# Kernel optimization log

Measured on AMD Instinct MI355X. Metric: run time of the kernel, lower is better.

Reference implementation:

```python
import jax, jax.numpy as jnp
import numpy as np

B, C, T = 4, 80, 800            # batch, n_mels (= d_model), frames
DEPTH, D_IN, N, DT_R, K = 12, 160, 16, 5, 4  # layers, expand*d_model, d_state, dt_rank, conv kernel
ATT, EMB, EPS = 128, 192, 1e-12

LP_NAMES = ['ln1_g','ln1_b','in_proj','conv_w','conv_b','x_proj','dt_w','dt_b','A_log','D','out_proj','ln2_g','ln2_b','ff_w1','ff_b1','ff_w2','ff_b2']
PP_NAMES = ['att_w1','att_b1','bn1_g','bn1_b','bn1_m','bn1_v','att_w2','att_b2','bn2_g','bn2_b','bn2_m','bn2_v','fc_w','fc_b']


def _layernorm(x, g, b, eps=1e-5):
    mu = x.mean(-1, keepdims=True)
    v = ((x - mu) ** 2).mean(-1, keepdims=True)
    return (x - mu) * jax.lax.rsqrt(v + eps) * g + b


def _mamba(x, p):
    # x: [B, L, d_model] -> standard Mamba selective-scan block
    xz = x @ p['in_proj']                              # [B,L,2*D_IN]
    xc, z = jnp.split(xz, 2, axis=-1)
    xp = jnp.pad(xc, ((0, 0), (K - 1, 0), (0, 0)))     # causal left pad
    xc = jax.lax.conv_general_dilated(
        xp, p['conv_w'], (1,), 'VALID',
        dimension_numbers=('NWC', 'WIO', 'NWC'),
        feature_group_count=D_IN) + p['conv_b']
    xc = jax.nn.silu(xc)
    dbc = xc @ p['x_proj']                             # [B,L,DT_R+2N]
    dt, Bm, Cm = jnp.split(dbc, [DT_R, DT_R + N], axis=-1)
    dt = jax.nn.softplus(dt @ p['dt_w'] + p['dt_b'])   # [B,L,D_IN]
    A = -jnp.exp(p['A_log'])                           # [D_IN,N]

    def step(h, inp):
        x_t, dt_t, B_t, C_t = inp                      # [B,D],[B,D],[B,N],[B,N]
        dA = jnp.exp(dt_t[..., None] * A)              # [B,D,N]
        h = dA * h + (dt_t * x_t)[..., None] * B_t[:, None, :]
        y = jnp.einsum('bdn,bn->bd', h, C_t)
        return h, y

    h0 = jnp.zeros((x.shape[0], D_IN, N), x.dtype)
    xs = tuple(jnp.swapaxes(a, 0, 1) for a in (xc, dt, Bm, Cm))
    _, ys = jax.lax.scan(step, h0, xs)
    y = jnp.swapaxes(ys, 0, 1) + xc * p['D']
    y = y * jax.nn.silu(z)
    return y @ p['out_proj']


def _encoder(x, p):
    xn = _layernorm(x, p['ln1_g'], p['ln1_b'])
    fwd = _mamba(xn, p)
    bwd = jnp.flip(_mamba(jnp.flip(xn, 1), p), 1)      # bidirectional, shared weights
    m = _layernorm(fwd + bwd, p['ln2_g'], p['ln2_b'])
    ff = jax.nn.gelu(m @ p['ff_w1'] + p['ff_b1'], approximate=False) @ p['ff_w2'] + p['ff_b2']
    return ff + x


def _forward(feat, lp, pp):
    feat = feat - feat.mean(-1, keepdims=True)         # CMN
    x = jnp.swapaxes(feat, 1, 2)                       # [B,T,C]

    def body(xc, p):
        return _encoder(xc, p), None

    x, _ = jax.lax.scan(body, x, lp)                   # 12 stacked layers
    x = jnp.swapaxes(x, 1, 2)                          # [B,C,T]

    # Attentive statistics pooling (global context)
    mean = x.mean(-1, keepdims=True)
    std = jnp.sqrt(jnp.maximum(((x - mean) ** 2).mean(-1, keepdims=True), EPS))
    g = jnp.concatenate([x, jnp.broadcast_to(mean, x.shape), jnp.broadcast_to(std, x.shape)], axis=1)  # [B,3C,T]
    a = jnp.einsum('bct,cd->bdt', g, pp['att_w1']) + pp['att_b1'][:, None]
    a = jax.nn.relu(a)
    a = (a - pp['bn1_m'][:, None]) * jax.lax.rsqrt(pp['bn1_v'][:, None] + 1e-5) * pp['bn1_g'][:, None] + pp['bn1_b'][:, None]
    a = jnp.tanh(a)
    a = jnp.einsum('bdt,dc->bct', a, pp['att_w2']) + pp['att_b2'][:, None]
    w = jax.nn.softmax(a, axis=-1)
    mu = jnp.sum(w * x, axis=-1)
    sg = jnp.sqrt(jnp.maximum(jnp.sum(w * x * x, axis=-1) - mu ** 2, EPS))
    pooled = jnp.concatenate([mu, sg], axis=-1)        # [B,2C]

    pooled = (pooled - pp['bn2_m']) * jax.lax.rsqrt(pp['bn2_v'] + 1e-5) * pp['bn2_g'] + pp['bn2_b']
    return pooled @ pp['fc_w'] + pp['fc_b']            # [B,EMB] source embedding


def setup_inputs() -> dict:
    key = jax.random.key(0)
    ks = jax.random.split(key, 12)

    def w(k, shape, s=0.05):
        return jax.random.normal(k, shape, jnp.float32) * s

    L = DEPTH
    return {
        'feat': jax.random.normal(ks[0], (B, C, T), jnp.float32),
        'ln1_g': jnp.ones((L, C)), 'ln1_b': jnp.zeros((L, C)),
        'in_proj': w(ks[1], (L, C, 2 * D_IN)),
        'conv_w': w(ks[2], (L, K, 1, D_IN), 0.2),
        'conv_b': jnp.zeros((L, D_IN)),
        'x_proj': w(ks[3], (L, D_IN, DT_R + 2 * N)),
        'dt_w': w(ks[4], (L, DT_R, D_IN), 0.2),
        'dt_b': jnp.full((L, D_IN), -2.0),
        'A_log': jnp.tile(jnp.log(jnp.arange(1, N + 1, dtype=jnp.float32)), (L, D_IN, 1)),
        'D': jnp.ones((L, D_IN)),
        'out_proj': w(ks[5], (L, D_IN, C)),
        'ln2_g': jnp.ones((L, C)), 'ln2_b': jnp.zeros((L, C)),
        'ff_w1': w(ks[6], (L, C, 4 * C)), 'ff_b1': jnp.zeros((L, 4 * C)),
        'ff_w2': w(ks[7], (L, 4 * C, C)), 'ff_b2': jnp.zeros((L, C)),
        'att_w1': w(ks[8], (3 * C, ATT)), 'att_b1': jnp.zeros((ATT,)),
        'bn1_g': jnp.ones((ATT,)), 'bn1_b': jnp.zeros((ATT,)),
        'bn1_m': jnp.zeros((ATT,)), 'bn1_v': jnp.ones((ATT,)),
        'att_w2': w(ks[9], (ATT, C)), 'att_b2': jnp.zeros((C,)),
        'bn2_g': jnp.ones((2 * C,)), 'bn2_b': jnp.zeros((2 * C,)),
        'bn2_m': jnp.zeros((2 * C,)), 'bn2_v': jnp.ones((2 * C,)),
        'fc_w': w(ks[10], (2 * C, EMB)), 'fc_b': jnp.zeros((EMB,)),
        'aug': 0,
    }


def reference(feat, ln1_g, ln1_b, in_proj, conv_w, conv_b, x_proj, dt_w, dt_b, A_log, D, out_proj, ln2_g, ln2_b, ff_w1, ff_b1, ff_w2, ff_b2, att_w1, att_b1, bn1_g, bn1_b, bn1_m, bn1_v, att_w2, att_b2, bn2_g, bn2_b, bn2_m, bn2_v, fc_w, fc_b, aug):
    lp = dict(zip(LP_NAMES, (ln1_g, ln1_b, in_proj, conv_w, conv_b, x_proj, dt_w, dt_b, A_log, D, out_proj, ln2_g, ln2_b, ff_w1, ff_b1, ff_w2, ff_b2)))
    pp = dict(zip(PP_NAMES, (att_w1, att_b1, bn1_g, bn1_b, bn1_m, bn1_v, att_w2, att_b2, bn2_g, bn2_b, bn2_m, bn2_v, fc_w, fc_b)))
    # aug == 0 -> SpecAug skipped (eval path); speaker branch (frozen, no_grad) omitted
    return _forward(feat, lp, pp)
```

## Files before the change

### kernel.cpp

```cpp
#include <hip/hip_runtime.h>
#include <hip/hip_bf16.h>

#define B_ 4
#define C_ 80
#define T_ 800
#define R_ 3200
#define DIN 160
#define NST 16
#define NC 16
#define LCH 50

typedef const float* fp;

__device__ __forceinline__ void g2l16(const float* g, float* l) {
  __builtin_amdgcn_global_load_lds(
      (const __attribute__((address_space(1))) void*)g,
      (__attribute__((address_space(3))) void*)l,
      16, 0, 0);
}

__device__ __forceinline__ float blockSum(float v, float* sb) {
  for (int o = 32; o; o >>= 1) v += __shfl_xor(v, o);
  __syncthreads();
  if ((threadIdx.x & 63) == 0) sb[threadIdx.x >> 6] = v;
  __syncthreads();
  return sb[0] + sb[1] + sb[2] + sb[3];
}
__device__ __forceinline__ float blockMax(float v, float* sb) {
  for (int o = 32; o; o >>= 1) v = fmaxf(v, __shfl_xor(v, o));
  __syncthreads();
  if ((threadIdx.x & 63) == 0) sb[threadIdx.x >> 6] = v;
  __syncthreads();
  return fmaxf(fmaxf(sb[0], sb[1]), fmaxf(sb[2], sb[3]));
}

__global__ __launch_bounds__(256) void prepw_k(fp in_proj, fp ff_w1,
    fp ln1_g, fp ln1_b, fp ln2_g, fp ln2_b, fp ff_b1,
    float* __restrict__ wp, float* __restrict__ uvb) {
  int idx = blockIdx.x * 256 + threadIdx.x;
  int c = idx % 320, lm = idx / 320;
  int mat = lm & 1, l = lm >> 1;
  fp W = (mat ? ff_w1 : in_proj) + l * 25600;
  fp g = (mat ? ln2_g : ln1_g) + l * 80;
  fp b = (mat ? ln2_b : ln1_b) + l * 80;
  float* wpo = wp + lm * 25600;
  float u = 0.f, v = 0.f;
  for (int k = 0; k < 80; ++k) {
    float w = W[k * 320 + c];
    float gw = g[k] * w;
    wpo[k * 320 + c] = gw;
    u += gw;
    v += b[k] * w;
  }
  if (mat) v += ff_b1[l * 320 + c];
  uvb[lm * 640 + c] = u;
  uvb[lm * 640 + 320 + c] = v;
}

__global__ __launch_bounds__(256) void prepx_k(fp x_proj, float* __restrict__ xpt) {
  int idx = blockIdx.x * 256 + threadIdx.x;
  if (idx >= 71040) return;
  int l = idx / 5920, r = idx % 5920;
  int c = r / 160, k = r % 160;
  xpt[idx] = x_proj[l * 5920 + k * 37 + c];
}

__global__ __launch_bounds__(256) void cmn_k(fp feat, float* __restrict__ x) {
  int bc = blockIdx.x;
  int b = bc / C_, c = bc % C_;
  const float* f = feat + (b * C_ + c) * T_;
  __shared__ float sb[4];
  int tid = threadIdx.x;
  float v[4]; float s = 0.f;
  #pragma unroll
  for (int i = 0; i < 4; ++i) {
    int t = tid + i * 256;
    v[i] = (t < T_) ? f[t] : 0.f;
    s += v[i];
  }
  s = blockSum(s, sb);
  float mu = s * (1.f / T_);
  #pragma unroll
  for (int i = 0; i < 4; ++i) {
    int t = tid + i * 256;
    if (t < T_) x[(b * T_ + t) * C_ + c] = v[i] - mu;
  }
}

__global__ __launch_bounds__(256) void rstat_k(const float* __restrict__ in,
                                               float* __restrict__ must) {
  int row = blockIdx.x * 16 + (threadIdx.x >> 4);
  int c16 = threadIdx.x & 15;
  float s = 0.f, q = 0.f;
  #pragma unroll
  for (int m = 0; m < 5; ++m) {
    float v = in[row * 80 + c16 + 16 * m];
    s += v; q += v * v;
  }
  s += __shfl_xor(s, 1); s += __shfl_xor(s, 2);
  s += __shfl_xor(s, 4); s += __shfl_xor(s, 8);
  q += __shfl_xor(q, 1); q += __shfl_xor(q, 2);
  q += __shfl_xor(q, 4); q += __shfl_xor(q, 8);
  if (c16 == 0) {
    float mu = s * 0.0125f;
    float rs = rsqrtf(fmaxf(q * 0.0125f - mu * mu, 0.f) + 1e-5f);
    must[row * 2] = mu;
    must[row * 2 + 1] = rs;
  }
}

template<int EPI>
__global__ __launch_bounds__(256, 4) void gw_k(const float* __restrict__ A,
    fp W, fp uv, const float* __restrict__ must, const float* __restrict__ extra,
    float* __restrict__ out, int N) {
  __shared__ float SL[5120 + 4 * 1280];
  int tid = threadIdx.x, wv = tid >> 6, ln = tid & 63;
  int bid = blockIdx.x;
  int c0 = (bid / 50) * 64;
  int row0 = ((bid % 50) * 4 + wv) * 16;
  for (int ch = wv; ch < 20; ch += 4) {
    int m = ch * 256 + ln * 4;
    int kr = m >> 6, cc = m & 63;
    int lo = __builtin_amdgcn_readfirstlane(ch * 256);
    g2l16(W + kr * N + c0 + cc, SL + lo);
  }
  int abase = __builtin_amdgcn_readfirstlane(5120 + wv * 1280);
  float* As = SL + 5120 + wv * 1280;
  #pragma unroll
  for (int i = 0; i < 5; ++i) {
    int m = i * 256 + ln * 4;
    int r = m / 80, kk = m - r * 80;
    g2l16(A + (row0 + r) * 80 + kk, SL + abase + i * 256);
  }
  __syncthreads();
  int rq = ln >> 4, c16 = ln & 15;
  float acc[4][4] = {};
  #pragma unroll 2
  for (int k4 = 0; k4 < 80; k4 += 4) {
    float4 a[4], w[4];
    #pragma unroll
    for (int i = 0; i < 4; ++i)
      a[i] = *(const float4*)&As[(rq * 4 + i) * 80 + k4];
    #pragma unroll
    for (int kk = 0; kk < 4; ++kk)
      w[kk] = *(const float4*)&SL[(k4 + kk) * 64 + c16 * 4];
    #pragma unroll
    for (int i = 0; i < 4; ++i) {
      acc[i][0] += a[i].x*w[0].x + a[i].y*w[1].x + a[i].z*w[2].x + a[i].w*w[3].x;
      acc[i][1] += a[i].x*w[0].y + a[i].y*w[1].y + a[i].z*w[2].y + a[i].w*w[3].y;
      acc[i][2] += a[i].x*w[0].z + a[i].y*w[1].z + a[i].z*w[2].z + a[i].w*w[3].z;
      acc[i][3] += a[i].x*w[0].w + a[i].y*w[1].w + a[i].z*w[2].w + a[i].w*w[3].w;
    }
  }
  float ua[4], va[4];
  if (EPI != 3) {
    *(float4*)ua = *(const float4*)&uv[c0 + c16 * 4];
    *(float4*)va = *(const float4*)&uv[N + c0 + c16 * 4];
  }
  #pragma unroll
  for (int i = 0; i < 4; ++i) {
    int row = row0 + rq * 4 + i;
    float mu = 0.f, rs = 1.f;
    if (EPI != 3) {
      float2 ms = *(const float2*)&must[row * 2];
      mu = ms.x; rs = ms.y;
    }
    float4 o;
    float* op = &o.x;
    #pragma unroll
    for (int j = 0; j < 4; ++j) {
      float v = acc[i][j];
      if (EPI == 3) {
        int c = c0 + c16 * 4 + j;
        v += extra[(row / T_) * 128 + c];
        v = fmaxf(v, 0.f);
        v = v * extra[512 + c] + extra[640 + c];
        v = tanhf(v);
      } else {
        v = rs * v - mu * rs * ua[j] + va[j];
        if (EPI == 1) v = 0.5f * v * (1.f + erff(v * 0.70710678118f));
      }
      op[j] = v;
    }
    *(float4*)&out[row * N + c0 + c16 * 4] = o;
  }
}

template<int EPI, int KCH, int NKC, int SUM2, int STAT>
__global__ __launch_bounds__(256, 4) void gc_k(const float* __restrict__ A,
    fp W, fp bias, const float* __restrict__ extra, float* __restrict__ out,
    int Astride, float* __restrict__ must) {
  constexpr int P = KCH + 4;
  __shared__ float As[16 * P];
  __shared__ float Wt[80 * P];
  int tid = threadIdx.x;
  int row0 = blockIdx.x * 16;
  int rr = tid >> 4, c16 = tid & 15;
  float acc[5] = {};
  for (int kc = 0; kc < NKC; ++kc) {
    if (kc) __syncthreads();
    #pragma unroll
    for (int i = 0; i < 16 * KCH / 256; ++i) {
      int e = tid + i * 256;
      int r = e / KCH, k = e - r * KCH;
      float v;
      if (SUM2) v = A[(row0 + r) * 320 + k] + A[(row0 + r) * 320 + 160 + k];
      else      v = A[(row0 + r) * Astride + kc * KCH + k];
      As[r * P + k] = v;
    }
    #pragma unroll
    for (int i = 0; i < KCH * 80 / 256; ++i) {
      int e = tid + i * 256;
      int kr = e / 80, c = e - kr * 80;
      Wt[c * P + kr] = W[(kc * KCH + kr) * 80 + c];
    }
    __syncthreads();
    #pragma unroll 4
    for (int k4 = 0; k4 < KCH; k4 += 4) {
      float4 a = *(const float4*)&As[rr * P + k4];
      #pragma unroll
      for (int m = 0; m < 5; ++m) {
        float4 w = *(const float4*)&Wt[(c16 + 16 * m) * P + k4];
        acc[m] += a.x * w.x + a.y * w.y + a.z * w.z + a.w * w.w;
      }
    }
  }
  int row = row0 + rr;
  float s = 0.f, q = 0.f;
  #pragma unroll
  for (int m = 0; m < 5; ++m) {
    int c = c16 + 16 * m;
    float v = acc[m];
    if (EPI == 2) v += bias[c] + extra[row * 80 + c];
    else if (EPI == 4) v += bias[c];
    out[row * 80 + c] = v;
    if (STAT) { s += v; q += v * v; }
  }
  if (STAT) {
    s += __shfl_xor(s, 1); s += __shfl_xor(s, 2);
    s += __shfl_xor(s, 4); s += __shfl_xor(s, 8);
    q += __shfl_xor(q, 1); q += __shfl_xor(q, 2);
    q += __shfl_xor(q, 4); q += __shfl_xor(q, 8);
    if (c16 == 0) {
      float mu = s * 0.0125f;
      float rs = rsqrtf(fmaxf(q * 0.0125f - mu * mu, 0.f) + 1e-5f);
      must[row * 2] = mu;
      must[row * 2 + 1] = rs;
    }
  }
}

__global__ __launch_bounds__(256) void cxf_k(const float* __restrict__ xz,
    fp cw, fp cb, fp xptl, fp dtw, fp dtb,
    float* __restrict__ xcf, float* __restrict__ xcbb,
    float* __restrict__ dbc2, float* __restrict__ dt2) {
  __shared__ float As[16 * 164];
  __shared__ float dbcl[16 * 40];
  int bi = blockIdx.x;
  int tc = bi % 50; int rem = bi / 50;
  int b = rem & 3, dir = rem >> 2;
  int t0 = tc * 16;
  int tid = threadIdx.x;
  float* xco = dir ? xcbb : xcf;
  #pragma unroll
  for (int i = 0; i < 3; ++i) {
    int e = tid + i * 256;
    if (e < 640) {
      int ii = e / 40, d4 = (e - ii * 40) * 4;
      int t = t0 + ii;
      float4 acc = *(const float4*)&cb[d4];
      #pragma unroll
      for (int k = 0; k < 4; ++k) {
        int tt = t - 3 + k;
        if (tt >= 0) {
          int src = dir ? (T_ - 1 - tt) : tt;
          float4 xv = *(const float4*)&xz[(b * T_ + src) * 320 + d4];
          float4 wv = *(const float4*)&cw[k * DIN + d4];
          acc.x += wv.x * xv.x; acc.y += wv.y * xv.y;
          acc.z += wv.z * xv.z; acc.w += wv.w * xv.w;
        }
      }
      float4 o;
      o.x = acc.x / (1.f + __expf(-acc.x));
      o.y = acc.y / (1.f + __expf(-acc.y));
      o.z = acc.z / (1.f + __expf(-acc.z));
      o.w = acc.w / (1.f + __expf(-acc.w));
      *(float4*)&As[ii * 164 + d4] = o;
      *(float4*)&xco[(b * T_ + t) * DIN + d4] = o;
    }
  }
  __syncthreads();
  int rr = tid >> 4, c16 = tid & 15;
  int grow0 = dir * R_ + b * T_ + t0;
  {
    float a0 = 0.f, a1 = 0.f, a2 = 0.f;
    for (int k4 = 0; k4 < 160; k4 += 4) {
      float4 a = *(const float4*)&As[rr * 164 + k4];
      float4 w0 = *(const float4*)&xptl[c16 * 160 + k4];
      float4 w1 = *(const float4*)&xptl[(c16 + 16) * 160 + k4];
      a0 += a.x * w0.x + a.y * w0.y + a.z * w0.z + a.w * w0.w;
      a1 += a.x * w1.x + a.y * w1.y + a.z * w1.z + a.w * w1.w;
      if (c16 < 5) {
        float4 w2 = *(const float4*)&xptl[(c16 + 32) * 160 + k4];
        a2 += a.x * w2.x + a.y * w2.y + a.z * w2.z + a.w * w2.w;
      }
    }
    dbcl[rr * 40 + c16] = a0;
    dbcl[rr * 40 + c16 + 16] = a1;
    dbc2[(grow0 + rr) * 37 + c16] = a0;
    dbc2[(grow0 + rr) * 37 + c16 + 16] = a1;
    if (c16 < 5) {
      dbcl[rr * 40 + c16 + 32] = a2;
      dbc2[(grow0 + rr) * 37 + c16 + 32] = a2;
    }
  }
  __syncthreads();
  #pragma unroll
  for (int i = 0; i < 10; ++i) {
    int e = tid + i * 256;
    int ii = e / 160, d = e - ii * 160;
    float v = dtb[d];
    #pragma unroll
    for (int m = 0; m < 5; ++m) v += dbcl[ii * 40 + m] * dtw[m * DIN + d];
    v = fmaxf(v, 0.f) + log1pf(expf(-fabsf(v)));
    dt2[(grow0 + ii) * DIN + d] = v;
  }
}

__global__ __launch_bounds__(256) void scanA_k(const float* __restrict__ dt2,
    const float* __restrict__ xcf, const float* __restrict__ xcbb,
    const float* __restrict__ dbc2, fp A_log,
    float* __restrict__ hend, float* __restrict__ pprod) {
  int bi = blockIdx.x;
  int cch = bi % NC; int rem = bi / NC;
  int dblk = rem % 10; rem /= 10;
  int b = rem % 4; int dir = rem / 4;
  int d0 = dblk * 16;
  int tid = threadIdx.x, dl = tid >> 4, n = tid & 15;
  int d = d0 + dl;
  float Areg = -__expf(A_log[d * NST + n]);
  __shared__ float sdt[LCH][16], sdx[LCH][16], sB[LCH][16];
  const float* xc = dir ? xcbb : xcf;
  int rbase = dir * R_ + b * T_ + cch * LCH;
  int rloc0 = b * T_ + cch * LCH;
  for (int e = tid; e < LCH * 16; e += 256) {
    int i = e >> 4, jj = e & 15;
    int grow = rbase + i;
    float dtv = dt2[grow * DIN + d0 + jj];
    sdt[i][jj] = dtv;
    sdx[i][jj] = dtv * xc[(rloc0 + i) * DIN + d0 + jj];
    sB[i][jj]  = dbc2[grow * 37 + 5 + jj];
  }
  __syncthreads();
  float h = 0.f, dts = 0.f;
  #pragma unroll 2
  for (int i = 0; i < LCH; ++i) {
    float dtv = sdt[i][dl];
    float a = __expf(dtv * Areg);
    h = a * h + sdx[i][dl] * sB[i][n];
    dts += dtv;
  }
  hend[bi * 256 + tid] = h;
  pprod[bi * 256 + tid] = __expf(dts * Areg);
}

__global__ __launch_bounds__(256) void scanC_k(const float* __restrict__ dt2,
    const float* __restrict__ dbc2, const float* __restrict__ xcf,
    const float* __restrict__ xcbb, const float* __restrict__ xz,
    fp A_log, fp Dp, const float* __restrict__ hend,
    const float* __restrict__ pprod, float* __restrict__ ygcat) {
  int bi = blockIdx.x;
  int cch = bi % NC; int rem = bi / NC;
  int dblk = rem % 10; rem /= 10;
  int b = rem % 4; int dir = rem / 4;
  int d0 = dblk * 16;
  int tid = threadIdx.x, dl = tid >> 4, n = tid & 15;
  int d = d0 + dl;
  float Areg = -__expf(A_log[d * NST + n]);
  __shared__ float sdt[LCH][16], sdx[LCH][16], sB[LCH][16], sC[LCH][16];
  __shared__ float sY[LCH][16];
  const float* xc = dir ? xcbb : xcf;
  int rbase = dir * R_ + b * T_ + cch * LCH;
  int rloc0 = b * T_ + cch * LCH;
  int sbase = (bi / NC) * (NC * 256) + tid;
  float h = 0.f;
  #pragma unroll
  for (int cc = 0; cc < NC; ++cc) {
    float p = pprod[sbase + cc * 256];
    float e = hend[sbase + cc * 256];
    if (cc < cch) h = p * h + e;
  }
  for (int e = tid; e < LCH * 16; e += 256) {
    int i = e >> 4, jj = e & 15;
    int grow = rbase + i;
    float dtv = dt2[grow * DIN + d0 + jj];
    sdt[i][jj] = dtv;
    sdx[i][jj] = dtv * xc[(rloc0 + i) * DIN + d0 + jj];
    sB[i][jj]  = dbc2[grow * 37 + 5 + jj];
    sC[i][jj]  = dbc2[grow * 37 + 21 + jj];
  }
  __syncthreads();
  for (int i = 0; i < LCH; ++i) {
    float a = __expf(sdt[i][dl] * Areg);
    h = a * h + sdx[i][dl] * sB[i][n];
    float y = h * sC[i][n];
    y += __shfl_xor(y, 1);
    y += __shfl_xor(y, 2);
    y += __shfl_xor(y, 4);
    y += __shfl_xor(y, 8);
    if (n == 0) sY[i][dl] = y;
  }
  __syncthreads();
  for (int e = tid; e < LCH * 16; e += 256) {
    int i = e >> 4, jj = e & 15;
    int t = cch * LCH + i;
    int rloc = b * T_ + t;
    float xcv = xc[rloc * DIN + d0 + jj];
    int orow = dir ? (b * T_ + (T_ - 1 - t)) : rloc;
    float z = xz[orow * 320 + 160 + d0 + jj];
    float sg = 1.f / (1.f + __expf(-z));
    ygcat[orow * 320 + dir * 160 + d0 + jj] = (sY[i][jj] + xcv * Dp[d0 + jj]) * (z * sg);
  }
}

__global__ __launch_bounds__(256) void stats_k(const float* __restrict__ x,
                                               float* __restrict__ meanv, float* __restrict__ stdv) {
  int bc = blockIdx.x; int b = bc / C_, c = bc % C_;
  __shared__ float sb[4];
  int tid = threadIdx.x;
  float v[4]; float s = 0.f;
  #pragma unroll
  for (int i = 0; i < 4; ++i) {
    int t = tid + i * 256;
    v[i] = (t < T_) ? x[(b * T_ + t) * C_ + c] : 0.f;
    s += v[i];
  }
  s = blockSum(s, sb);
  float mu = s * (1.f / T_);
  float q = 0.f;
  #pragma unroll
  for (int i = 0; i < 4; ++i) {
    int t = tid + i * 256;
    if (t < T_) { float dd = v[i] - mu; q += dd * dd; }
  }
  q = blockSum(q, sb);
  if (tid == 0) { meanv[bc] = mu; stdv[bc] = sqrtf(fmaxf(q * (1.f / T_), 1e-12f)); }
}

__global__ __launch_bounds__(256) void prep_k(const float* __restrict__ meanv,
    const float* __restrict__ stdv, fp w1, fp ab1, fp g1p, fp b1p, fp m1p, fp v1p,
    float* __restrict__ pack) {
  int idx = blockIdx.x * 256 + threadIdx.x;
  if (idx < 512) {
    int b = idx / 128, dcol = idx % 128;
    float acc = ab1[dcol];
    for (int c = 0; c < C_; ++c) {
      acc += meanv[b * C_ + c] * w1[(C_ + c) * 128 + dcol];
      acc += stdv[b * C_ + c] * w1[(2 * C_ + c) * 128 + dcol];
    }
    pack[idx] = acc;
  } else if (idx < 640) {
    int dcol = idx - 512;
    float kv = g1p[dcol] * rsqrtf(v1p[dcol] + 1e-5f);
    pack[512 + dcol] = kv;
    pack[640 + dcol] = b1p[dcol] - m1p[dcol] * kv;
  }
}

__global__ __launch_bounds__(256) void pool_k(const float* __restrict__ x,
    const float* __restrict__ scores, fp g2, fp b2, fp m2, fp v2,
    float* __restrict__ pooledn) {
  int bc = blockIdx.x; int b = bc / C_, c = bc % C_;
  __shared__ float sb[4];
  int tid = threadIdx.x;
  float sv[4], xv[4];
  float mx = -1e30f;
  #pragma unroll
  for (int i = 0; i < 4; ++i) {
    int t = tid + i * 256;
    if (t < T_) { sv[i] = scores[(b * T_ + t) * C_ + c]; xv[i] = x[(b * T_ + t) * C_ + c]; }
    else { sv[i] = -1e30f; xv[i] = 0.f; }
    mx = fmaxf(mx, sv[i]);
  }
  mx = blockMax(mx, sb);
  float se = 0.f, sx = 0.f, sxx = 0.f;
  #pragma unroll
  for (int i = 0; i < 4; ++i) {
    float e = expf(sv[i] - mx);
    se += e; sx += e * xv[i]; sxx += e * xv[i] * xv[i];
  }
  se = blockSum(se, sb);
  sx = blockSum(sx, sb);
  sxx = blockSum(sxx, sb);
  if (tid == 0) {
    float mu = sx / se;
    float sg = sqrtf(fmaxf(sxx / se - mu * mu, 1e-12f));
    int j0 = c, j1 = C_ + c;
    pooledn[b * 160 + j0] = (mu - m2[j0]) * rsqrtf(v2[j0] + 1e-5f) * g2[j0] + b2[j0];
    pooledn[b * 160 + j1] = (sg - m2[j1]) * rsqrtf(v2[j1] + 1e-5f) * g2[j1] + b2[j1];
  }
}

__global__ __launch_bounds__(256) void fc_k(const float* __restrict__ pooledn, fp fw, fp fb,
                                            float* __restrict__ out) {
  int idx = blockIdx.x * 256 + threadIdx.x;
  if (idx >= 4 * 192) return;
  int b = idx / 192, e = idx % 192;
  float acc = fb[e];
  for (int i = 0; i < 160; ++i) acc += pooledn[b * 160 + i] * fw[i * 192 + e];
  out[idx] = acc;
}

extern "C" void kernel_launch(void* const* d_in, const int* in_sizes, int n_in,
                              void* d_out, int out_size, void* d_ws, size_t ws_size,
                              hipStream_t stream) {
  fp feat   = (fp)d_in[0];
  fp ln1_g  = (fp)d_in[1];  fp ln1_b  = (fp)d_in[2];
  fp in_proj= (fp)d_in[3];
  fp conv_w = (fp)d_in[4];  fp conv_b = (fp)d_in[5];
  fp x_proj = (fp)d_in[6];
  fp dt_w   = (fp)d_in[7];  fp dt_b   = (fp)d_in[8];
  fp A_log  = (fp)d_in[9];  fp Dp     = (fp)d_in[10];
  fp out_proj=(fp)d_in[11];
  fp ln2_g  = (fp)d_in[12]; fp ln2_b  = (fp)d_in[13];
  fp ff_w1  = (fp)d_in[14]; fp ff_b1  = (fp)d_in[15];
  fp ff_w2  = (fp)d_in[16]; fp ff_b2  = (fp)d_in[17];
  fp att_w1 = (fp)d_in[18]; fp att_b1 = (fp)d_in[19];
  fp bn1_g  = (fp)d_in[20]; fp bn1_b  = (fp)d_in[21];
  fp bn1_m  = (fp)d_in[22]; fp bn1_v  = (fp)d_in[23];
  fp att_w2 = (fp)d_in[24]; fp att_b2 = (fp)d_in[25];
  fp bn2_g  = (fp)d_in[26]; fp bn2_b  = (fp)d_in[27];
  fp bn2_m  = (fp)d_in[28]; fp bn2_v  = (fp)d_in[29];
  fp fc_w   = (fp)d_in[30]; fp fc_b   = (fp)d_in[31];

  float* ws   = (float*)d_ws;
  float* x    = ws;
  float* xz   = ws + 256000;
  float* xcf  = ws + 1280000;
  float* xcb  = ws + 1792000;
  float* dbc2 = ws + 2304000;
  float* dt2  = ws + 2540800;
  float* hend = ws + 3564800;
  float* pprod= ws + 3892480;
  float* ygcat= ws + 4220160;
  float* sbuf = ws + 5244160;
  float* meanv= ws + 5500160;
  float* stdv = ws + 5500480;
  float* pack = ws + 5500800;
  float* pooledn = ws + 5501568;
  float* wp   = ws + 5502208;
  float* uvb  = ws + 6116608;
  float* mst_x= ws + 6131968;
  float* mst_s= ws + 6138368;
  float* xpt  = ws + 6144768;
  float* g1   = xz;
  float* a1b  = hend;
  float* sc   = dt2;

  prepw_k<<<30, 256, 0, stream>>>(in_proj, ff_w1, ln1_g, ln1_b, ln2_g, ln2_b,
                                  ff_b1, wp, uvb);
  prepx_k<<<278, 256, 0, stream>>>(x_proj, xpt);
  cmn_k<<<320, 256, 0, stream>>>(feat, x);
  rstat_k<<<200, 256, 0, stream>>>(x, mst_x);

  for (int l = 0; l < 12; ++l) {
    gw_k<0><<<250, 256, 0, stream>>>(x, wp + (2 * l) * 25600, uvb + (2 * l) * 640,
                                     mst_x, nullptr, xz, 320);
    cxf_k<<<400, 256, 0, stream>>>(xz, conv_w + l * 640, conv_b + l * 160,
                                   xpt + l * 5920, dt_w + l * 800, dt_b + l * 160,
                                   xcf, xcb, dbc2, dt2);
    scanA_k<<<1280, 256, 0, stream>>>(dt2, xcf, xcb, dbc2, A_log + l * 2560, hend, pprod);
    scanC_k<<<1280, 256, 0, stream>>>(dt2, dbc2, xcf, xcb, xz, A_log + l * 2560,
                                      Dp + l * 160, hend, pprod, ygcat);
    gc_k<0, 160, 1, 1, 1><<<200, 256, 0, stream>>>(ygcat, out_proj + l * 12800,
                                                   nullptr, nullptr, sbuf, 320, mst_s);
    gw_k<1><<<250, 256, 0, stream>>>(sbuf, wp + (2 * l + 1) * 25600,
                                     uvb + (2 * l + 1) * 640, mst_s, nullptr, g1, 320);
    gc_k<2, 160, 2, 0, 1><<<200, 256, 0, stream>>>(g1, ff_w2 + l * 25600,
                                                   ff_b2 + l * 80, x, x, 320, mst_x);
  }

  stats_k<<<320, 256, 0, stream>>>(x, meanv, stdv);
  prep_k<<<3, 256, 0, stream>>>(meanv, stdv, att_w1, att_b1, bn1_g, bn1_b, bn1_m, bn1_v, pack);
  gw_k<3><<<100, 256, 0, stream>>>(x, att_w1, nullptr, nullptr, pack, a1b, 128);
  gc_k<4, 128, 1, 0, 0><<<200, 256, 0, stream>>>(a1b, att_w2, att_b2, nullptr, sc, 128, nullptr);
  pool_k<<<320, 256, 0, stream>>>(x, sc, bn2_g, bn2_b, bn2_m, bn2_v, pooledn);
  fc_k<<<3, 256, 0, stream>>>(pooledn, fc_w, fc_b, (float*)d_out);
}
```

Measured before the change: 1.377 ms.

## Fuse per-layer GEMM chain into two kernels and stage x_proj weights in LDS

Replaces the per-layer out_proj, ff_w1 and ff_w2 plus next-layer in_proj kernels with two fused kernels. gof_k runs out_proj, LayerNorm2 statistics and ff_w1 with GELU. gfi_k runs ff_w2 with the residual, LayerNorm1 statistics and the next layer's in_proj, so intermediate rows and statistics stay in LDS. This cuts launches and global round-trips. Weights are pre-transposed once up front, cxf_k stages the x_proj weights in shared memory, and the softplus now uses fast intrinsics. In exchange the fused kernels use large LDS tiles at lower occupancy, and there is a small precision change in softplus.

```diff
diff --git a/kernel.cpp b/kernel.cpp
--- a/kernel.cpp
+++ b/kernel.cpp
@@ -65,6 +65,21 @@
   xpt[idx] = x_proj[l * 5920 + k * 37 + c];
 }
 
+__global__ __launch_bounds__(256) void prept_k(fp out_proj, fp ff_w2,
+    float* __restrict__ wot, float* __restrict__ w2t) {
+  int idx = blockIdx.x * 256 + threadIdx.x;
+  if (idx < 153600) {
+    int l = idx / 12800, r = idx % 12800;
+    int c = r / 160, k = r % 160;
+    wot[idx] = out_proj[l * 12800 + k * 80 + c];
+  } else if (idx < 153600 + 307200) {
+    int j = idx - 153600;
+    int l = j / 25600, r = j % 25600;
+    int c = r / 320, k = r % 320;
+    w2t[j] = ff_w2[l * 25600 + k * 80 + c];
+  }
+}
+
 __global__ __launch_bounds__(256) void cmn_k(fp feat, float* __restrict__ x) {
   int bc = blockIdx.x;
   int b = bc / C_, c = bc % C_;
@@ -178,7 +193,6 @@
         v = tanhf(v);
       } else {
         v = rs * v - mu * rs * ua[j] + va[j];
-        if (EPI == 1) v = 0.5f * v * (1.f + erff(v * 0.70710678118f));
       }
       op[j] = v;
     }
@@ -226,7 +240,6 @@
     }
   }
   int row = row0 + rr;
-  float s = 0.f, q = 0.f;
   #pragma unroll
   for (int m = 0; m < 5; ++m) {
     int c = c16 + 16 * m;
@@ -234,18 +247,158 @@
     if (EPI == 2) v += bias[c] + extra[row * 80 + c];
     else if (EPI == 4) v += bias[c];
     out[row * 80 + c] = v;
-    if (STAT) { s += v; q += v * v; }
-  }
-  if (STAT) {
+  }
+}
+
+__global__ __launch_bounds__(256, 2) void gof_k(const float* __restrict__ yg,
+    fp wotl, fp w1pl, fp uv1, float* __restrict__ g1) {
+  __shared__ float As[16 * 164];
+  __shared__ float Wt[80 * 164];
+  __shared__ float sl[16 * 84];
+  __shared__ float ss[32];
+  int tid = threadIdx.x, row0 = blockIdx.x * 16, rr = tid >> 4, c16 = tid & 15;
+  #pragma unroll
+  for (int i = 0; i < 10; ++i) {
+    int e = tid + i * 256; int r = e / 160, k = e - r * 160;
+    As[r * 164 + k] = yg[(row0 + r) * 320 + k] + yg[(row0 + r) * 320 + 160 + k];
+  }
+  #pragma unroll
+  for (int i = 0; i < 50; ++i) {
+    int e = tid + i * 256; int c = e / 160, k = e - c * 160;
+    Wt[c * 164 + k] = wotl[e];
+  }
+  __syncthreads();
+  float acc[5] = {};
+  #pragma unroll 4
+  for (int k4 = 0; k4 < 160; k4 += 4) {
+    float4 a = *(const float4*)&As[rr * 164 + k4];
+    #pragma unroll
+    for (int m = 0; m < 5; ++m) {
+      float4 w = *(const float4*)&Wt[(c16 + 16 * m) * 164 + k4];
+      acc[m] += a.x * w.x + a.y * w.y + a.z * w.z + a.w * w.w;
+    }
+  }
+  float s = 0.f, q = 0.f;
+  #pragma unroll
+  for (int m = 0; m < 5; ++m) {
+    float v = acc[m];
+    sl[rr * 84 + c16 + 16 * m] = v;
+    s += v; q += v * v;
+  }
+  s += __shfl_xor(s, 1); s += __shfl_xor(s, 2);
+  s += __shfl_xor(s, 4); s += __shfl_xor(s, 8);
+  q += __shfl_xor(q, 1); q += __shfl_xor(q, 2);
+  q += __shfl_xor(q, 4); q += __shfl_xor(q, 8);
+  if (c16 == 0) {
+    float mu = s * 0.0125f;
+    ss[rr * 2] = mu;
+    ss[rr * 2 + 1] = rsqrtf(fmaxf(q * 0.0125f - mu * mu, 0.f) + 1e-5f);
+  }
+  for (int h = 0; h < 2; ++h) {
+    __syncthreads();
+    #pragma unroll
+    for (int i = 0; i < 50; ++i) {
+      int e = tid + i * 256; int kr = e / 160, c = e - kr * 160;
+      Wt[kr * 164 + c] = w1pl[kr * 320 + h * 160 + c];
+    }
+    __syncthreads();
+    float mu = ss[rr * 2], rs = ss[rr * 2 + 1];
+    float a2[10] = {};
+    for (int k = 0; k < 80; k += 4) {
+      float4 av = *(const float4*)&sl[rr * 84 + k];
+      #pragma unroll
+      for (int m = 0; m < 10; ++m) {
+        int c = c16 + 16 * m;
+        a2[m] += av.x * Wt[k * 164 + c] + av.y * Wt[(k + 1) * 164 + c]
+               + av.z * Wt[(k + 2) * 164 + c] + av.w * Wt[(k + 3) * 164 + c];
+      }
+    }
+    #pragma unroll
+    for (int m = 0; m < 10; ++m) {
+      int c = h * 160 + c16 + 16 * m;
+      float v = rs * a2[m] - mu * rs * uv1[c] + uv1[320 + c];
+      v = 0.5f * v * (1.f + erff(v * 0.70710678118f));
+      g1[(row0 + rr) * 320 + c] = v;
+    }
+  }
+}
+
+template<int LAST>
+__global__ __launch_bounds__(256, 2) void gfi_k(const float* __restrict__ g1,
+    fp w2tl, fp fb2, float* __restrict__ x, fp wpn, fp uvn,
+    float* __restrict__ xz) {
+  __shared__ float As[16 * 164];
+  __shared__ float Wt[80 * 164];
+  __shared__ float xn[16 * 84];
+  __shared__ float ss[32];
+  int tid = threadIdx.x, row0 = blockIdx.x * 16, rr = tid >> 4, c16 = tid & 15;
+  float acc[5] = {};
+  for (int kc = 0; kc < 2; ++kc) {
+    if (kc) __syncthreads();
+    #pragma unroll
+    for (int i = 0; i < 10; ++i) {
+      int e = tid + i * 256; int r = e / 160, k = e - r * 160;
+      As[r * 164 + k] = g1[(row0 + r) * 320 + kc * 160 + k];
+    }
+    #pragma unroll
+    for (int i = 0; i < 50; ++i) {
+      int e = tid + i * 256; int c = e / 160, k = e - c * 160;
+      Wt[c * 164 + k] = w2tl[c * 320 + kc * 160 + k];
+    }
+    __syncthreads();
+    #pragma unroll 4
+    for (int k4 = 0; k4 < 160; k4 += 4) {
+      float4 a = *(const float4*)&As[rr * 164 + k4];
+      #pragma unroll
+      for (int m = 0; m < 5; ++m) {
+        float4 w = *(const float4*)&Wt[(c16 + 16 * m) * 164 + k4];
+        acc[m] += a.x * w.x + a.y * w.y + a.z * w.z + a.w * w.w;
+      }
+    }
+  }
+  float s = 0.f, q = 0.f;
+  #pragma unroll
+  for (int m = 0; m < 5; ++m) {
+    int c = c16 + 16 * m;
+    float v = acc[m] + fb2[c] + x[(row0 + rr) * 80 + c];
+    x[(row0 + rr) * 80 + c] = v;
+    xn[rr * 84 + c] = v;
+    s += v; q += v * v;
+  }
+  if (!LAST) {
     s += __shfl_xor(s, 1); s += __shfl_xor(s, 2);
     s += __shfl_xor(s, 4); s += __shfl_xor(s, 8);
     q += __shfl_xor(q, 1); q += __shfl_xor(q, 2);
     q += __shfl_xor(q, 4); q += __shfl_xor(q, 8);
     if (c16 == 0) {
       float mu = s * 0.0125f;
-      float rs = rsqrtf(fmaxf(q * 0.0125f - mu * mu, 0.f) + 1e-5f);
-      must[row * 2] = mu;
-      must[row * 2 + 1] = rs;
+      ss[rr * 2] = mu;
+      ss[rr * 2 + 1] = rsqrtf(fmaxf(q * 0.0125f - mu * mu, 0.f) + 1e-5f);
+    }
+    for (int h = 0; h < 2; ++h) {
+      __syncthreads();
+      #pragma unroll
+      for (int i = 0; i < 50; ++i) {
+        int e = tid + i * 256; int kr = e / 160, c = e - kr * 160;
+        Wt[kr * 164 + c] = wpn[kr * 320 + h * 160 + c];
+      }
+      __syncthreads();
+      float mu = ss[rr * 2], rs = ss[rr * 2 + 1];
+      float a2[10] = {};
+      for (int k = 0; k < 80; k += 4) {
+        float4 av = *(const float4*)&xn[rr * 84 + k];
+        #pragma unroll
+        for (int m = 0; m < 10; ++m) {
+          int c = c16 + 16 * m;
+          a2[m] += av.x * Wt[k * 164 + c] + av.y * Wt[(k + 1) * 164 + c]
+                 + av.z * Wt[(k + 2) * 164 + c] + av.w * Wt[(k + 3) * 164 + c];
+        }
+      }
+      #pragma unroll
+      for (int m = 0; m < 10; ++m) {
+        int c = h * 160 + c16 + 16 * m;
+        xz[(row0 + rr) * 320 + c] = rs * a2[m] - mu * rs * uvn[c] + uvn[320 + c];
+      }
     }
   }
 }
@@ -255,12 +408,21 @@
     float* __restrict__ xcf, float* __restrict__ xcbb,
     float* __restrict__ dbc2, float* __restrict__ dt2) {
   __shared__ float As[16 * 164];
+  __shared__ float xpT[37 * 164];
   __shared__ float dbcl[16 * 40];
   int bi = blockIdx.x;
   int tc = bi % 50; int rem = bi / 50;
   int b = rem & 3, dir = rem >> 2;
   int t0 = tc * 16;
   int tid = threadIdx.x;
+  #pragma unroll
+  for (int i = 0; i < 24; ++i) {
+    int e = tid + i * 256;
+    if (e < 5920) {
+      int c = e / 160, k = e - c * 160;
+      xpT[c * 164 + k] = xptl[e];
+    }
+  }
   float* xco = dir ? xcbb : xcf;
   #pragma unroll
   for (int i = 0; i < 3; ++i) {
@@ -296,12 +458,12 @@
     float a0 = 0.f, a1 = 0.f, a2 = 0.f;
     for (int k4 = 0; k4 < 160; k4 += 4) {
       float4 a = *(const float4*)&As[rr * 164 + k4];
-      float4 w0 = *(const float4*)&xptl[c16 * 160 + k4];
-      float4 w1 = *(const float4*)&xptl[(c16 + 16) * 160 + k4];
+      float4 w0 = *(const float4*)&xpT[c16 * 164 + k4];
+      float4 w1 = *(const float4*)&xpT[(c16 + 16) * 164 + k4];
       a0 += a.x * w0.x + a.y * w0.y + a.z * w0.z + a.w * w0.w;
       a1 += a.x * w1.x + a.y * w1.y + a.z * w1.z + a.w * w1.w;
       if (c16 < 5) {
-        float4 w2 = *(const float4*)&xptl[(c16 + 32) * 160 + k4];
+        float4 w2 = *(const float4*)&xpT[(c16 + 32) * 164 + k4];
         a2 += a.x * w2.x + a.y * w2.y + a.z * w2.z + a.w * w2.w;
       }
     }
@@ -322,7 +484,7 @@
     float v = dtb[d];
     #pragma unroll
     for (int m = 0; m < 5; ++m) v += dbcl[ii * 40 + m] * dtw[m * DIN + d];
-    v = fmaxf(v, 0.f) + log1pf(expf(-fabsf(v)));
+    v = fmaxf(v, 0.f) + __logf(1.f + __expf(-fabsf(v)));
     dt2[(grow0 + ii) * DIN + d] = v;
   }
 }
@@ -543,16 +705,16 @@
   float* hend = ws + 3564800;
   float* pprod= ws + 3892480;
   float* ygcat= ws + 4220160;
-  float* sbuf = ws + 5244160;
-  float* meanv= ws + 5500160;
-  float* stdv = ws + 5500480;
-  float* pack = ws + 5500800;
-  float* pooledn = ws + 5501568;
-  float* wp   = ws + 5502208;
-  float* uvb  = ws + 6116608;
-  float* mst_x= ws + 6131968;
-  float* mst_s= ws + 6138368;
-  float* xpt  = ws + 6144768;
+  float* meanv= ws + 5244160;
+  float* stdv = ws + 5244480;
+  float* pack = ws + 5244800;
+  float* pooledn = ws + 5245568;
+  float* wp   = ws + 5246208;
+  float* uvb  = ws + 5860608;
+  float* mst_x= ws + 5875968;
+  float* xpt  = ws + 5882368;
+  float* wot  = ws + 5953408;
+  float* w2t  = ws + 6107008;
   float* g1   = xz;
   float* a1b  = hend;
   float* sc   = dt2;
@@ -560,24 +722,27 @@
   prepw_k<<<30, 256, 0, stream>>>(in_proj, ff_w1, ln1_g, ln1_b, ln2_g, ln2_b,
                                   ff_b1, wp, uvb);
   prepx_k<<<278, 256, 0, stream>>>(x_proj, xpt);
+  prept_k<<<1800, 256, 0, stream>>>(out_proj, ff_w2, wot, w2t);
   cmn_k<<<320, 256, 0, stream>>>(feat, x);
   rstat_k<<<200, 256, 0, stream>>>(x, mst_x);
+  gw_k<0><<<250, 256, 0, stream>>>(x, wp, uvb, mst_x, nullptr, xz, 320);
 
   for (int l = 0; l < 12; ++l) {
-    gw_k<0><<<250, 256, 0, stream>>>(x, wp + (2 * l) * 25600, uvb + (2 * l) * 640,
-                                     mst_x, nullptr, xz, 320);
     cxf_k<<<400, 256, 0, stream>>>(xz, conv_w + l * 640, conv_b + l * 160,
                                    xpt + l * 5920, dt_w + l * 800, dt_b + l * 160,
                                    xcf, xcb, dbc2, dt2);
     scanA_k<<<1280, 256, 0, stream>>>(dt2, xcf, xcb, dbc2, A_log + l * 2560, hend, pprod);
     scanC_k<<<1280, 256, 0, stream>>>(dt2, dbc2, xcf, xcb, xz, A_log + l * 2560,
                                       Dp + l * 160, hend, pprod, ygcat);
-    gc_k<0, 160, 1, 1, 1><<<200, 256, 0, stream>>>(ygcat, out_proj + l * 12800,
-                                                   nullptr, nullptr, sbuf, 320, mst_s);
-    gw_k<1><<<250, 256, 0, stream>>>(sbuf, wp + (2 * l + 1) * 25600,
-                                     uvb + (2 * l + 1) * 640, mst_s, nullptr, g1, 320);
-    gc_k<2, 160, 2, 0, 1><<<200, 256, 0, stream>>>(g1, ff_w2 + l * 25600,
-                                                   ff_b2 + l * 80, x, x, 320, mst_x);
+    gof_k<<<200, 256, 0, stream>>>(ygcat, wot + l * 12800, wp + (2 * l + 1) * 25600,
+                                   uvb + (2 * l + 1) * 640, g1);
+    if (l < 11)
+      gfi_k<0><<<200, 256, 0, stream>>>(g1, w2t + l * 25600, ff_b2 + l * 80, x,
+                                        wp + (2 * l + 2) * 25600,
+                                        uvb + (2 * l + 2) * 640, xz);
+    else
+      gfi_k<1><<<200, 256, 0, stream>>>(g1, w2t + l * 25600, ff_b2 + l * 80, x,
+                                        wp, uvb, xz);
   }
 
   stats_k<<<320, 256, 0, stream>>>(x, meanv, stdv);
```

Result: faster. 1.262 ms (-8.4%).
